# Optimization experiments

Hardware: AMD Instinct MI355X
Metric: run time of the kernel (lower is better)

The kernel has to match this reference:

```python
import jax, jax.numpy as jnp
import numpy as np

B, S, DMODEL, HEADS = 2, 2048, 1024, 16
DK = DMODEL // HEADS
DV = DMODEL // HEADS


def setup_inputs() -> dict:
    key = jax.random.key(0)
    kx, kq, kk, kv = jax.random.split(key, 4)
    x = jax.random.normal(kx, (B, S, DMODEL), dtype=jnp.float32)
    # stacked per-head projection weights, shape [H, dmodel, dk/dv]
    # (equivalent to nn.Linear(dmodel, dk, bias=False) per head)
    scale = 1.0 / np.sqrt(DMODEL)
    Wq = jax.random.uniform(kq, (HEADS, DMODEL, DK), jnp.float32, -scale, scale)
    Wk = jax.random.uniform(kk, (HEADS, DMODEL, DK), jnp.float32, -scale, scale)
    Wv = jax.random.uniform(kv, (HEADS, DMODEL, DV), jnp.float32, -scale, scale)
    return {"x": x, "Wq": Wq, "Wk": Wk, "Wv": Wv}


def reference(x, Wq, Wk, Wv):
    # per-head projections, batched across heads: [B,H,S,dk]
    q = jnp.einsum("bsd,hdk->bhsk", x, Wq)
    k = jnp.einsum("bsd,hdk->bhsk", x, Wk)
    v = jnp.einsum("bsd,hdv->bhsv", x, Wv)
    # NOTE: original module applies NO 1/sqrt(dk) scaling — keep faithful
    scores = jnp.einsum("bhqk,bhsk->bhqs", q, k)  # [B,H,S,S]
    attn = jax.nn.softmax(scores, axis=-1)
    out = jnp.einsum("bhqs,bhsv->bhqv", attn, v)  # [B,H,S,dv]
    # concat heads along last dim in head order
    Bsz, H, Sq, Dv = out.shape
    return jnp.transpose(out, (0, 2, 1, 3)).reshape(Bsz, Sq, H * Dv)
```

## Files before the change

kernel.cpp:

```cpp
#include <hip/hip_runtime.h>

#define B_ 2
#define S_ 2048
#define D_ 1024
#define H_ 16
#define DK_ 64
#define M_ (B_ * S_)
#define N_ (3 * D_)

typedef __bf16 bf16x8 __attribute__((ext_vector_type(8)));
typedef short s8vec __attribute__((ext_vector_type(8)));
typedef float f4vec __attribute__((ext_vector_type(4)));

static __device__ __forceinline__ ushort f2b(float f) {
  union { float f; unsigned u; } v; v.f = f;
  unsigned u = v.u;
  u += 0x7FFFu + ((u >> 16) & 1u);
  return (ushort)(u >> 16);
}

static __device__ __forceinline__ unsigned pk2(float a, float b) {
#if __has_builtin(__builtin_amdgcn_cvt_pk_bf16_f32)
  typedef __bf16 b2 __attribute__((ext_vector_type(2)));
  b2 r = __builtin_amdgcn_cvt_pk_bf16_f32(a, b);
  return __builtin_bit_cast(unsigned, r);
#else
  return (unsigned)f2b(a) | ((unsigned)f2b(b) << 16);
#endif
}

static __device__ __forceinline__ f4vec mfma16(s8vec a, s8vec b, f4vec c) {
  return __builtin_amdgcn_mfma_f32_16x16x32_bf16(
      __builtin_bit_cast(bf16x8, a), __builtin_bit_cast(bf16x8, b), c, 0, 0, 0);
}

static __device__ __forceinline__ void gl_lds16(const ushort* g, ushort* l) {
  __builtin_amdgcn_global_load_lds(
      (const __attribute__((address_space(1))) unsigned*)g,
      (__attribute__((address_space(3))) unsigned*)l, 16, 0, 0);
}

static __device__ __forceinline__ void wg_barrier_lds() {
  asm volatile("" ::: "memory");
  __builtin_amdgcn_s_waitcnt(0xC07F);
  __builtin_amdgcn_s_barrier();
  asm volatile("" ::: "memory");
}

__global__ void cvt_x(const float* __restrict__ x, ushort* __restrict__ xb) {
  int i = blockIdx.x * 256 + threadIdx.x;
  float4 v = ((const float4*)x)[i];
  ushort4 o;
  o.x = f2b(v.x); o.y = f2b(v.y); o.z = f2b(v.z); o.w = f2b(v.w);
  ((ushort4*)xb)[i] = o;
}

__global__ __launch_bounds__(256) void cvt_w(const float* __restrict__ Wq,
                                             const float* __restrict__ Wk,
                                             const float* __restrict__ Wv,
                                             ushort* __restrict__ wbt) {
  __shared__ ushort T[64 * 72];
  const int w = blockIdx.z, h = blockIdx.y, d0 = blockIdx.x * 64;
  const float* W = (w == 0) ? Wq : (w == 1) ? Wk : Wv;
  const float* src = W + (size_t)h * 65536 + (size_t)d0 * 64;
  const int t = threadIdx.x;
#pragma unroll
  for (int j = 0; j < 4; ++j) {
    int idx = j * 256 + t;
    int dr = idx >> 4, kc = (idx & 15) * 4;
    float4 v = *(const float4*)(src + dr * 64 + kc);
    T[(kc + 0) * 72 + dr] = f2b(v.x);
    T[(kc + 1) * 72 + dr] = f2b(v.y);
    T[(kc + 2) * 72 + dr] = f2b(v.z);
    T[(kc + 3) * 72 + dr] = f2b(v.w);
  }
  __syncthreads();
  const int kk = t >> 2, dcg = (t & 3) * 16;
  ushort* dst = wbt + ((size_t)w * 1024 + h * 64 + kk) * 1024 + d0 + dcg;
  *(s8vec*)dst       = *(const s8vec*)&T[kk * 72 + dcg];
  *(s8vec*)(dst + 8) = *(const s8vec*)&T[kk * 72 + dcg + 8];
}

__global__ __launch_bounds__(256) void proj_gemm(const ushort* __restrict__ xb,
                                                 const ushort* __restrict__ wbt,
                                                 ushort* __restrict__ qkv) {
  __shared__ __attribute__((aligned(16))) ushort As[128 * 64];
  __shared__ __attribute__((aligned(16))) ushort Bs[128 * 64];
  const int tid = threadIdx.x, wid = tid >> 6, lane = tid & 63;
  const int quad = lane >> 4, l15 = lane & 15;
  const int wm = wid & 1, wn = wid >> 1;
  const int m0 = blockIdx.x * 128, n0 = blockIdx.y * 128;

  f4vec acc[4][4];
#pragma unroll
  for (int mb = 0; mb < 4; mb++)
#pragma unroll
    for (int nb = 0; nb < 4; nb++)
#pragma unroll
      for (int i = 0; i < 4; i++) acc[mb][nb][i] = 0.f;

  const int sr = tid >> 3, sg = tid & 7;
  const int lg = sg ^ (sr & 7);
  const ushort* Ab = xb + (size_t)m0 * D_;
  const ushort* Bb = wbt + (size_t)n0 * D_;

  for (int k0 = 0; k0 < D_; k0 += 64) {
    __syncthreads();
#pragma unroll
    for (int j = 0; j < 4; ++j) {
      int r = j * 32 + sr;
      gl_lds16(Ab + (size_t)r * D_ + k0 + lg * 8, &As[j * 2048 + wid * 512]);
      gl_lds16(Bb + (size_t)r * D_ + k0 + lg * 8, &Bs[j * 2048 + wid * 512]);
    }
    __syncthreads();

#pragma unroll
    for (int kb = 0; kb < 2; ++kb) {
      s8vec af[4], bf[4];
#pragma unroll
      for (int mb = 0; mb < 4; ++mb) {
        int m = wm * 64 + mb * 16 + l15;
        int gpos = (kb * 4 + quad) ^ (m & 7);
        af[mb] = *(const s8vec*)&As[m * 64 + gpos * 8];
      }
#pragma unroll
      for (int nb = 0; nb < 4; ++nb) {
        int n = wn * 64 + nb * 16 + l15;
        int gpos = (kb * 4 + quad) ^ (n & 7);
        bf[nb] = *(const s8vec*)&Bs[n * 64 + gpos * 8];
      }
#pragma unroll
      for (int mb = 0; mb < 4; ++mb)
#pragma unroll
        for (int nb = 0; nb < 4; ++nb)
          acc[mb][nb] = mfma16(af[mb], bf[nb], acc[mb][nb]);
    }
  }

  const size_t per = (size_t)B_ * H_ * S_ * DK_;
  const int w = n0 >> 10;
  if (w == 2) {
    ushort* vt = qkv + 2 * per;
#pragma unroll
    for (int mb = 0; mb < 4; ++mb)
#pragma unroll
      for (int nb = 0; nb < 4; ++nb)
#pragma unroll
        for (int i = 0; i < 4; ++i) {
          int m = m0 + wm * 64 + mb * 16 + quad * 4 + i;
          int b = m >> 11, s = m & 2047;
          int n1 = (n0 & 1023) + wn * 64 + nb * 16 + l15;
          vt[((size_t)b * 1024 + n1) * S_ + s] = f2b(acc[mb][nb][i]);
        }
  } else {
#pragma unroll
    for (int mb = 0; mb < 4; ++mb)
#pragma unroll
      for (int nb = 0; nb < 4; ++nb)
#pragma unroll
        for (int i = 0; i < 4; ++i) {
          int m = m0 + wm * 64 + mb * 16 + quad * 4 + i;
          int b = m >> 11, s = m & 2047;
          int n1 = (n0 & 1023) + wn * 64 + nb * 16 + l15;
          qkv[(size_t)w * per + (((size_t)b * H_ + (n1 >> 6)) * S_ + s) * 64 + (n1 & 63)] =
              f2b(acc[mb][nb][i]);
        }
  }
}

__global__ __launch_bounds__(512) void attn(const ushort* __restrict__ qg,
                                            const ushort* __restrict__ kg,
                                            const ushort* __restrict__ vtg,
                                            float* __restrict__ out) {
  __shared__ __attribute__((aligned(16))) ushort Ks[128 * 64];
  __shared__ __attribute__((aligned(16))) ushort Vt[2][64 * 64];
  __shared__ __attribute__((aligned(16))) ushort Ps[8][16 * 132];
  const int qt = blockIdx.x, bh = blockIdx.y;
  const int b = bh >> 4, h = bh & 15;
  const int tid = threadIdx.x, wid = tid >> 6, lane = tid & 63;
  const int quad = lane >> 4, l15 = lane & 15, l7 = l15 & 7;

  const ushort* qbase = qg + ((size_t)bh * S_ + qt * 128 + wid * 16) * DK_;
  s8vec aq0 = *(const s8vec*)(qbase + (size_t)l15 * DK_ + quad * 8);
  s8vec aq1 = *(const s8vec*)(qbase + (size_t)l15 * DK_ + 32 + quad * 8);

  f4vec o[4];
  float lsum[4];
#pragma unroll
  for (int i = 0; i < 4; i++) {
    lsum[i] = 0.f;
#pragma unroll
    for (int nb = 0; nb < 4; nb++) o[nb][i] = 0.f;
  }

  const int r = tid >> 3, gs = tid & 7;
  const int gk = gs ^ (r & 7);
  const ushort* kb_ = kg + (size_t)bh * S_ * DK_;
  const ushort* vb_ = vtg + (size_t)bh * 64 * S_ + (size_t)r * S_;

  s8vec kr0 = *(const s8vec*)(kb_ + (size_t)r * DK_ + gk * 8);
  s8vec kr1 = *(const s8vec*)(kb_ + (size_t)(64 + r) * DK_ + gk * 8);
  s8vec vr0 = *(const s8vec*)(vb_ + gk * 8);
  s8vec vr1 = *(const s8vec*)(vb_ + 64 + gk * 8);

  for (int kt = 0; kt < S_ / 128; ++kt) {
    wg_barrier_lds();
    *(s8vec*)&Ks[r * 64 + gs * 8]        = kr0;
    *(s8vec*)&Ks[(64 + r) * 64 + gs * 8] = kr1;
    *(s8vec*)&Vt[0][r * 64 + gs * 8]     = vr0;
    *(s8vec*)&Vt[1][r * 64 + gs * 8]     = vr1;
    if (kt + 1 < S_ / 128) {
      const ushort* kn = kb_ + (size_t)((kt + 1) * 128 + r) * DK_ + gk * 8;
      kr0 = *(const s8vec*)(kn);
      kr1 = *(const s8vec*)(kn + (size_t)64 * DK_);
      const ushort* vn = vb_ + (kt + 1) * 128 + gk * 8;
      vr0 = *(const s8vec*)(vn);
      vr1 = *(const s8vec*)(vn + 64);
    }
    wg_barrier_lds();

    f4vec sc[8];
#pragma unroll
    for (int nb = 0; nb < 8; nb++) {
#pragma unroll
      for (int i = 0; i < 4; i++) sc[nb][i] = 0.f;
      const int row = nb * 16 + l15;
      s8vec bk0 = *(const s8vec*)&Ks[row * 64 + ((0 + quad) ^ l7) * 8];
      s8vec bk1 = *(const s8vec*)&Ks[row * 64 + ((4 + quad) ^ l7) * 8];
      sc[nb] = mfma16(aq0, bk0, sc[nb]);
      sc[nb] = mfma16(aq1, bk1, sc[nb]);
    }

#pragma unroll
    for (int nb = 0; nb < 8; nb++) {
#pragma unroll
      for (int i = 0; i < 4; i++) {
        float p = __expf(sc[nb][i]);
        sc[nb][i] = p;
        lsum[i] += p;
      }
      unsigned p01 = pk2(sc[nb][0], sc[nb][1]);
      unsigned p23 = pk2(sc[nb][2], sc[nb][3]);
      ushort* pw = &Ps[wid][quad * 4 * 132 + nb * 16 + l15];
      pw[0]   = (ushort)p01;
      pw[132] = (ushort)(p01 >> 16);
      pw[264] = (ushort)p23;
      pw[396] = (ushort)(p23 >> 16);
    }

#pragma unroll
    for (int kb2 = 0; kb2 < 4; kb2++) {
      s8vec ap = *(const s8vec*)(&Ps[wid][l15 * 132 + kb2 * 32 + quad * 8]);
      const int half = kb2 >> 1, G = (kb2 & 1) * 4 + quad;
#pragma unroll
      for (int nb = 0; nb < 4; nb++) {
        s8vec bv = *(const s8vec*)&Vt[half][(nb * 16 + l15) * 64 + (G ^ l7) * 8];
        o[nb] = mfma16(ap, bv, o[nb]);
      }
    }
  }

#pragma unroll
  for (int i = 0; i < 4; i++) {
#pragma unroll
    for (int msk = 1; msk < 16; msk <<= 1) lsum[i] += __shfl_xor(lsum[i], msk, 64);
  }

  float* ob = out + ((size_t)b * S_ + qt * 128 + wid * 16) * D_ + h * DK_;
#pragma unroll
  for (int i = 0; i < 4; i++) {
    float inv = 1.0f / lsum[i];
#pragma unroll
    for (int nb = 0; nb < 4; nb++)
      ob[(size_t)(quad * 4 + i) * D_ + nb * 16 + l15] = o[nb][i] * inv;
  }
}

extern "C" void kernel_launch(void* const* d_in, const int* in_sizes, int n_in,
                              void* d_out, int out_size, void* d_ws, size_t ws_size,
                              hipStream_t stream) {
  const float* x  = (const float*)d_in[0];
  const float* Wq = (const float*)d_in[1];
  const float* Wk = (const float*)d_in[2];
  const float* Wv = (const float*)d_in[3];
  float* out = (float*)d_out;

  ushort* xb  = (ushort*)d_ws;
  ushort* wbt = xb + (size_t)B_ * S_ * D_;
  ushort* qkv = wbt + (size_t)3 * D_ * D_;
  const size_t per = (size_t)B_ * H_ * S_ * DK_;

  cvt_x<<<(B_ * S_ * D_) / 4 / 256, 256, 0, stream>>>(x, xb);
  cvt_w<<<dim3(16, 16, 3), 256, 0, stream>>>(Wq, Wk, Wv, wbt);
  proj_gemm<<<dim3(M_ / 128, N_ / 128), 256, 0, stream>>>(xb, wbt, qkv);
  attn<<<dim3(S_ / 128, B_ * H_), 512, 0, stream>>>(qkv, qkv + per, qkv + 2 * per, out);
}
```

Measured before the change: 174.9 us.

## Compute transposed scores in registers and feed P to PV via permlane swaps

The attention kernel now computes S^T (K as the A operand, Q as B), so the exp'd probabilities can be repacked into MFMA operand layout with v_permlane16/32 swaps rather than being staged through a per-wave LDS buffer. Each wave handles 32 query rows with 256 threads per block, which halves the number of waves sharing each K/V tile. The log2(e) factor is folded into Wq during weight conversion so the kernel can call the hardware exp2. Output stores become float4 writes. This removes LDS round trips and their bank traffic for P, at the cost of higher register pressure and reliance on gfx950-only permlane swap instructions.

```diff
diff --git a/kernel.cpp b/kernel.cpp
--- a/kernel.cpp
+++ b/kernel.cpp
@@ -29,6 +29,14 @@
 #endif
 }
 
+static __device__ __forceinline__ float exp2f_fast(float x) {
+#if __has_builtin(__builtin_amdgcn_exp2f)
+  return __builtin_amdgcn_exp2f(x);
+#else
+  return __expf(x * 0.6931471805599453f);
+#endif
+}
+
 static __device__ __forceinline__ f4vec mfma16(s8vec a, s8vec b, f4vec c) {
   return __builtin_amdgcn_mfma_f32_16x16x32_bf16(
       __builtin_bit_cast(bf16x8, a), __builtin_bit_cast(bf16x8, b), c, 0, 0, 0);
@@ -62,6 +70,7 @@
   __shared__ ushort T[64 * 72];
   const int w = blockIdx.z, h = blockIdx.y, d0 = blockIdx.x * 64;
   const float* W = (w == 0) ? Wq : (w == 1) ? Wk : Wv;
+  const float sc = (w == 0) ? 1.4426950408889634f : 1.0f;
   const float* src = W + (size_t)h * 65536 + (size_t)d0 * 64;
   const int t = threadIdx.x;
 #pragma unroll
@@ -69,10 +78,10 @@
     int idx = j * 256 + t;
     int dr = idx >> 4, kc = (idx & 15) * 4;
     float4 v = *(const float4*)(src + dr * 64 + kc);
-    T[(kc + 0) * 72 + dr] = f2b(v.x);
-    T[(kc + 1) * 72 + dr] = f2b(v.y);
-    T[(kc + 2) * 72 + dr] = f2b(v.z);
-    T[(kc + 3) * 72 + dr] = f2b(v.w);
+    T[(kc + 0) * 72 + dr] = f2b(v.x * sc);
+    T[(kc + 1) * 72 + dr] = f2b(v.y * sc);
+    T[(kc + 2) * 72 + dr] = f2b(v.z * sc);
+    T[(kc + 3) * 72 + dr] = f2b(v.w * sc);
   }
   __syncthreads();
   const int kk = t >> 2, dcg = (t & 3) * 16;
@@ -168,112 +177,142 @@
   }
 }
 
-__global__ __launch_bounds__(512) void attn(const ushort* __restrict__ qg,
+__global__ __launch_bounds__(256) void attn(const ushort* __restrict__ qg,
                                             const ushort* __restrict__ kg,
                                             const ushort* __restrict__ vtg,
                                             float* __restrict__ out) {
   __shared__ __attribute__((aligned(16))) ushort Ks[128 * 64];
   __shared__ __attribute__((aligned(16))) ushort Vt[2][64 * 64];
-  __shared__ __attribute__((aligned(16))) ushort Ps[8][16 * 132];
   const int qt = blockIdx.x, bh = blockIdx.y;
   const int b = bh >> 4, h = bh & 15;
   const int tid = threadIdx.x, wid = tid >> 6, lane = tid & 63;
   const int quad = lane >> 4, l15 = lane & 15, l7 = l15 & 7;
 
-  const ushort* qbase = qg + ((size_t)bh * S_ + qt * 128 + wid * 16) * DK_;
-  s8vec aq0 = *(const s8vec*)(qbase + (size_t)l15 * DK_ + quad * 8);
-  s8vec aq1 = *(const s8vec*)(qbase + (size_t)l15 * DK_ + 32 + quad * 8);
-
-  f4vec o[4];
-  float lsum[4];
-#pragma unroll
-  for (int i = 0; i < 4; i++) {
-    lsum[i] = 0.f;
-#pragma unroll
-    for (int nb = 0; nb < 4; nb++) o[nb][i] = 0.f;
-  }
-
-  const int r = tid >> 3, gs = tid & 7;
-  const int gk = gs ^ (r & 7);
+  const ushort* qbase = qg + ((size_t)bh * S_ + qt * 128 + wid * 32) * DK_;
+  s8vec bq[2][2];
+#pragma unroll
+  for (int qb = 0; qb < 2; ++qb)
+#pragma unroll
+    for (int kc = 0; kc < 2; ++kc)
+      bq[qb][kc] = *(const s8vec*)(qbase + (size_t)(qb * 16 + l15) * DK_ + kc * 32 + quad * 8);
+
+  f4vec o[4][2];
+  float lsum[2] = {0.f, 0.f};
+#pragma unroll
+  for (int nb = 0; nb < 4; ++nb)
+#pragma unroll
+    for (int qb = 0; qb < 2; ++qb)
+#pragma unroll
+      for (int i = 0; i < 4; ++i) o[nb][qb][i] = 0.f;
+
+  const int r5 = tid >> 3, gs = tid & 7;
+  const int gk = gs ^ (r5 & 7);
   const ushort* kb_ = kg + (size_t)bh * S_ * DK_;
-  const ushort* vb_ = vtg + (size_t)bh * 64 * S_ + (size_t)r * S_;
-
-  s8vec kr0 = *(const s8vec*)(kb_ + (size_t)r * DK_ + gk * 8);
-  s8vec kr1 = *(const s8vec*)(kb_ + (size_t)(64 + r) * DK_ + gk * 8);
-  s8vec vr0 = *(const s8vec*)(vb_ + gk * 8);
-  s8vec vr1 = *(const s8vec*)(vb_ + 64 + gk * 8);
+  const ushort* vb_ = vtg + (size_t)bh * 64 * S_;
+
+  s8vec kr[4], vr[4];
+#pragma unroll
+  for (int j = 0; j < 4; ++j)
+    kr[j] = *(const s8vec*)(kb_ + (size_t)(j * 32 + r5) * DK_ + gk * 8);
+#pragma unroll
+  for (int jd = 0; jd < 2; ++jd)
+#pragma unroll
+    for (int hf = 0; hf < 2; ++hf)
+      vr[jd * 2 + hf] = *(const s8vec*)(vb_ + (size_t)(jd * 32 + r5) * S_ + hf * 64 + gk * 8);
 
   for (int kt = 0; kt < S_ / 128; ++kt) {
     wg_barrier_lds();
-    *(s8vec*)&Ks[r * 64 + gs * 8]        = kr0;
-    *(s8vec*)&Ks[(64 + r) * 64 + gs * 8] = kr1;
-    *(s8vec*)&Vt[0][r * 64 + gs * 8]     = vr0;
-    *(s8vec*)&Vt[1][r * 64 + gs * 8]     = vr1;
+#pragma unroll
+    for (int j = 0; j < 4; ++j)
+      *(s8vec*)&Ks[(j * 32 + r5) * 64 + gs * 8] = kr[j];
+#pragma unroll
+    for (int jd = 0; jd < 2; ++jd)
+#pragma unroll
+      for (int hf = 0; hf < 2; ++hf)
+        *(s8vec*)&Vt[hf][(jd * 32 + r5) * 64 + gs * 8] = vr[jd * 2 + hf];
     if (kt + 1 < S_ / 128) {
-      const ushort* kn = kb_ + (size_t)((kt + 1) * 128 + r) * DK_ + gk * 8;
-      kr0 = *(const s8vec*)(kn);
-      kr1 = *(const s8vec*)(kn + (size_t)64 * DK_);
-      const ushort* vn = vb_ + (kt + 1) * 128 + gk * 8;
-      vr0 = *(const s8vec*)(vn);
-      vr1 = *(const s8vec*)(vn + 64);
+      const ushort* kn = kb_ + (size_t)(kt + 1) * 128 * DK_;
+#pragma unroll
+      for (int j = 0; j < 4; ++j)
+        kr[j] = *(const s8vec*)(kn + (size_t)(j * 32 + r5) * DK_ + gk * 8);
+      const ushort* vn = vb_ + (kt + 1) * 128;
+#pragma unroll
+      for (int jd = 0; jd < 2; ++jd)
+#pragma unroll
+        for (int hf = 0; hf < 2; ++hf)
+          vr[jd * 2 + hf] = *(const s8vec*)(vn + (size_t)(jd * 32 + r5) * S_ + hf * 64 + gk * 8);
     }
     wg_barrier_lds();
 
-    f4vec sc[8];
-#pragma unroll
-    for (int nb = 0; nb < 8; nb++) {
-#pragma unroll
-      for (int i = 0; i < 4; i++) sc[nb][i] = 0.f;
-      const int row = nb * 16 + l15;
-      s8vec bk0 = *(const s8vec*)&Ks[row * 64 + ((0 + quad) ^ l7) * 8];
-      s8vec bk1 = *(const s8vec*)&Ks[row * 64 + ((4 + quad) ^ l7) * 8];
-      sc[nb] = mfma16(aq0, bk0, sc[nb]);
-      sc[nb] = mfma16(aq1, bk1, sc[nb]);
-    }
-
-#pragma unroll
-    for (int nb = 0; nb < 8; nb++) {
-#pragma unroll
-      for (int i = 0; i < 4; i++) {
-        float p = __expf(sc[nb][i]);
-        sc[nb][i] = p;
-        lsum[i] += p;
+#pragma unroll
+    for (int kc2 = 0; kc2 < 4; ++kc2) {
+      s8vec ak[2][2];
+#pragma unroll
+      for (int kbs = 0; kbs < 2; ++kbs) {
+        const int row = (kc2 * 2 + kbs) * 16 + l15;
+        ak[kbs][0] = *(const s8vec*)&Ks[row * 64 + ((0 + quad) ^ l7) * 8];
+        ak[kbs][1] = *(const s8vec*)&Ks[row * 64 + ((4 + quad) ^ l7) * 8];
       }
-      unsigned p01 = pk2(sc[nb][0], sc[nb][1]);
-      unsigned p23 = pk2(sc[nb][2], sc[nb][3]);
-      ushort* pw = &Ps[wid][quad * 4 * 132 + nb * 16 + l15];
-      pw[0]   = (ushort)p01;
-      pw[132] = (ushort)(p01 >> 16);
-      pw[264] = (ushort)p23;
-      pw[396] = (ushort)(p23 >> 16);
-    }
-
-#pragma unroll
-    for (int kb2 = 0; kb2 < 4; kb2++) {
-      s8vec ap = *(const s8vec*)(&Ps[wid][l15 * 132 + kb2 * 32 + quad * 8]);
-      const int half = kb2 >> 1, G = (kb2 & 1) * 4 + quad;
-#pragma unroll
-      for (int nb = 0; nb < 4; nb++) {
-        s8vec bv = *(const s8vec*)&Vt[half][(nb * 16 + l15) * 64 + (G ^ l7) * 8];
-        o[nb] = mfma16(ap, bv, o[nb]);
+      const int half = kc2 >> 1, G = (kc2 & 1) * 4 + quad;
+      s8vec av[4];
+#pragma unroll
+      for (int nb = 0; nb < 4; ++nb)
+        av[nb] = *(const s8vec*)&Vt[half][(nb * 16 + l15) * 64 + ((G) ^ l7) * 8];
+
+      f4vec st[2][2];
+#pragma unroll
+      for (int kbs = 0; kbs < 2; ++kbs)
+#pragma unroll
+        for (int qb = 0; qb < 2; ++qb) {
+          f4vec z;
+#pragma unroll
+          for (int i = 0; i < 4; ++i) z[i] = 0.f;
+          z = mfma16(ak[kbs][0], bq[qb][0], z);
+          st[kbs][qb] = mfma16(ak[kbs][1], bq[qb][1], z);
+        }
+
+#pragma unroll
+      for (int qb = 0; qb < 2; ++qb) {
+        float p0 = exp2f_fast(st[0][qb][0]), p1 = exp2f_fast(st[0][qb][1]);
+        float p2 = exp2f_fast(st[0][qb][2]), p3 = exp2f_fast(st[0][qb][3]);
+        float p4 = exp2f_fast(st[1][qb][0]), p5 = exp2f_fast(st[1][qb][1]);
+        float p6 = exp2f_fast(st[1][qb][2]), p7 = exp2f_fast(st[1][qb][3]);
+        lsum[qb] += ((p0 + p1) + (p2 + p3)) + ((p4 + p5) + (p6 + p7));
+        unsigned w0 = pk2(p0, p1), w1 = pk2(p2, p3);
+        unsigned w2 = pk2(p4, p5), w3 = pk2(p6, p7);
+        asm("v_permlane32_swap_b32 %0, %1" : "+v"(w0), "+v"(w2));
+        asm("v_permlane16_swap_b32 %0, %1" : "+v"(w0), "+v"(w2));
+        asm("v_permlane32_swap_b32 %0, %1" : "+v"(w1), "+v"(w3));
+        asm("v_permlane16_swap_b32 %0, %1" : "+v"(w1), "+v"(w3));
+        union { unsigned u[4]; s8vec v; } pb;
+        pb.u[0] = w0; pb.u[1] = w1; pb.u[2] = w2; pb.u[3] = w3;
+#pragma unroll
+        for (int nb = 0; nb < 4; ++nb) o[nb][qb] = mfma16(av[nb], pb.v, o[nb][qb]);
       }
     }
   }
 
-#pragma unroll
-  for (int i = 0; i < 4; i++) {
-#pragma unroll
-    for (int msk = 1; msk < 16; msk <<= 1) lsum[i] += __shfl_xor(lsum[i], msk, 64);
-  }
-
-  float* ob = out + ((size_t)b * S_ + qt * 128 + wid * 16) * D_ + h * DK_;
-#pragma unroll
-  for (int i = 0; i < 4; i++) {
-    float inv = 1.0f / lsum[i];
-#pragma unroll
-    for (int nb = 0; nb < 4; nb++)
-      ob[(size_t)(quad * 4 + i) * D_ + nb * 16 + l15] = o[nb][i] * inv;
-  }
+  float inv[2];
+#pragma unroll
+  for (int qb = 0; qb < 2; ++qb) {
+    float s = lsum[qb];
+    s += __shfl_xor(s, 16, 64);
+    s += __shfl_xor(s, 32, 64);
+    inv[qb] = 1.0f / s;
+  }
+
+  float* ob = out + ((size_t)b * S_ + qt * 128 + wid * 32) * D_ + h * DK_;
+#pragma unroll
+  for (int qb = 0; qb < 2; ++qb)
+#pragma unroll
+    for (int nb = 0; nb < 4; ++nb) {
+      float4 vvv;
+      vvv.x = o[nb][qb][0] * inv[qb];
+      vvv.y = o[nb][qb][1] * inv[qb];
+      vvv.z = o[nb][qb][2] * inv[qb];
+      vvv.w = o[nb][qb][3] * inv[qb];
+      *(float4*)&ob[(size_t)(qb * 16 + l15) * D_ + nb * 16 + quad * 4] = vvv;
+    }
 }
 
 extern "C" void kernel_launch(void* const* d_in, const int* in_sizes, int n_in,
@@ -293,5 +332,5 @@
   cvt_x<<<(B_ * S_ * D_) / 4 / 256, 256, 0, stream>>>(x, xb);
   cvt_w<<<dim3(16, 16, 3), 256, 0, stream>>>(Wq, Wk, Wv, wbt);
   proj_gemm<<<dim3(M_ / 128, N_ / 128), 256, 0, stream>>>(xb, wbt, qkv);
-  attn<<<dim3(S_ / 128, B_ * H_), 512, 0, stream>>>(qkv, qkv + per, qkv + 2 * per, out);
-}
+  attn<<<dim3(S_ / 128, B_ * H_), 256, 0, stream>>>(qkv, qkv + per, qkv + 2 * per, out);
+}
```

Result: no change. 172.9 us (-1.1%).
